# Kernel optimization log

Hardware: AMD Instinct MI355X
Metric: run time of the kernel (lower is better)

The kernel has to match this reference:

```python
import jax, jax.numpy as jnp
import numpy as np

RRELU_SLOPE = (1.0 / 8.0 + 1.0 / 3.0) / 2.0  # F.rrelu deterministic (eval) slope

N_ENTS, H_DIM, R2, T, E = 50000, 200, 500, 4, 400000


def setup_inputs() -> dict:
    key = jax.random.key(0)
    ks = jax.random.split(key, 16)
    s = 0.05
    inp = {
        # learned parameters
        "dynamic_emb": jax.random.normal(ks[0], (N_ENTS, H_DIM), jnp.float32),
        "emb_rel": jax.random.normal(ks[1], (R2, H_DIM), jnp.float32) * s,
        "W_ih": jax.random.normal(ks[2], (3 * H_DIM, 2 * H_DIM), jnp.float32) * s,
        "W_hh": jax.random.normal(ks[3], (3 * H_DIM, H_DIM), jnp.float32) * s,
        "b_ih": jnp.zeros((3 * H_DIM,), jnp.float32),
        "b_hh": jnp.zeros((3 * H_DIM,), jnp.float32),
        "weight_neighbor": jax.random.normal(ks[4], (H_DIM, H_DIM), jnp.float32) * s,
        "time_gate_weight": jax.random.normal(ks[5], (H_DIM, H_DIM), jnp.float32) * s,
        "time_gate_bias": jnp.zeros((H_DIM,), jnp.float32),
        # per-timestep graph structure [T, E]
        "src": jax.random.randint(ks[6], (T, E), 0, N_ENTS, jnp.int32),
        "dst": jax.random.randint(ks[7], (T, E), 0, N_ENTS, jnp.int32),
        "etype": jax.random.randint(ks[8], (T, E), 0, R2, jnp.int32),
        "r_to_e": jax.random.randint(ks[9], (T, E), 0, N_ENTS, jnp.int32),
        "r_seg": jnp.sort(jax.random.randint(ks[10], (T, E), 0, R2, jnp.int32), axis=1),
    }
    return inp


def _l2norm(x):
    # torch F.normalize along dim=1
    return x / jnp.maximum(jnp.linalg.norm(x, axis=1, keepdims=True), 1e-12)


def reference(dynamic_emb, emb_rel, W_ih, W_hh, b_ih, b_hh, weight_neighbor,
              time_gate_weight, time_gate_bias, src, dst, etype, r_to_e, r_seg):
    N, H = dynamic_emb.shape
    R2_ = emb_rel.shape[0]

    def gru(x, hprev):
        gi = x @ W_ih.T + b_ih
        gh = hprev @ W_hh.T + b_hh
        ir, iz, inn = jnp.split(gi, 3, axis=1)
        hr, hz, hn = jnp.split(gh, 3, axis=1)
        r = jax.nn.sigmoid(ir + hr)
        z = jax.nn.sigmoid(iz + hz)
        n = jnp.tanh(inn + r * hn)
        return (1.0 - z) * n + z * hprev

    def rgcn(h, s, d, et):
        # UnionRGCNLayer: msg = (h_src + rel_emb[etype]) @ W_neighbor, sum-agg, 1/deg norm, rrelu
        msg = (h[s] + emb_rel[et]) @ weight_neighbor  # [E, H]
        agg = jax.ops.segment_sum(msg, d, num_segments=N)
        deg = jax.ops.segment_sum(jnp.ones((s.shape[0],), h.dtype), d, num_segments=N)
        norm = jnp.where(deg > 0, 1.0 / jnp.maximum(deg, 1.0), 0.0)
        out = agg * norm[:, None]
        return jnp.where(out >= 0, out, RRELU_SLOPE * out)

    h_init = _l2norm(dynamic_emb)  # layer_norm=True

    def step(carry, g):
        h, h0 = carry
        s, d, et, rte, rseg = g
        # ragged per-relation segment mean of entity embeddings
        temp = h[rte]  # [E, H]
        sums = jax.ops.segment_sum(temp, rseg, num_segments=R2_)
        cnts = jax.ops.segment_sum(jnp.ones((rte.shape[0],), h.dtype), rseg, num_segments=R2_)
        x_input = jnp.where(cnts[:, None] > 0, sums / jnp.maximum(cnts, 1.0)[:, None], 0.0)
        x_cat = jnp.concatenate([emb_rel, x_input], axis=1)  # [R2, 2H]
        h0_new = _l2norm(gru(x_cat, h0))
        cur = _l2norm(rgcn(h, s, d, et))
        tw = jax.nn.sigmoid(h @ time_gate_weight + time_gate_bias)
        h_new = _l2norm(tw * cur + (1.0 - tw) * h)
        return (h_new, h0_new), h_new

    (h_fin, h0_fin), evolve = jax.lax.scan(
        step, (h_init, emb_rel), (src, dst, etype, r_to_e, r_seg))
    return evolve, h0_fin  # evolve: [T, N, H]; h0: [2*num_rels, H]
```

## Files before the change

kernel.cpp:

```cpp
#include <hip/hip_runtime.h>
#include <hip/hip_bf16.h>

using bf16 = __hip_bfloat16;

constexpr int NE  = 50000;
constexpr int H   = 200;
constexpr int R2C = 500;
constexpr int TS  = 4;
constexpr int EC  = 400000;
constexpr float SLOPE = 0.22916666666666666f;
constexpr int NSCAN = (NE + 255) / 256;

constexpr int KP = 224;
constexpr int KS = 7;
constexpr int NT = 13;

constexpr int GNT = 38;
constexpr int GKI = 13;
constexpr int GKH = 7;
constexpr int GR  = 512;
constexpr int GCS = 608;

constexpr int RCH = 64;

#define DEVINL __device__ __forceinline__

typedef __bf16 bf16x8v __attribute__((ext_vector_type(8)));
typedef float  f32x4   __attribute__((ext_vector_type(4)));

DEVINL float b2f(bf16 v) { return __bfloat162float(v); }
DEVINL bf16  f2b(float v) { return __float2bfloat16(v); }
DEVINL unsigned short f2bu(float x) { bf16 b = f2b(x); return *reinterpret_cast<unsigned short*>(&b); }
DEVINL float u2f(unsigned short u) { unsigned int w = (unsigned int)u << 16; float f; __builtin_memcpy(&f, &w, 4); return f; }

DEVINL float wave_sum(float v) {
  #pragma unroll
  for (int o = 32; o > 0; o >>= 1) v += __shfl_xor(v, o, 64);
  return v;
}

DEVINL float sigmoidf(float x) { return 1.0f / (1.0f + expf(-x)); }

__global__ __launch_bounds__(256) void k_init_h(const float* __restrict__ de,
                                                float* __restrict__ h,
                                                unsigned short* __restrict__ hb0) {
  int wid = threadIdx.x >> 6, lane = threadIdx.x & 63;
  int row = blockIdx.x * 4 + wid;
  if (row >= NE) return;
  int d0 = lane * 4;
  bool act = d0 < H;
  float4 v = make_float4(0.f, 0.f, 0.f, 0.f);
  if (act) v = *reinterpret_cast<const float4*>(de + (size_t)row * H + d0);
  float ss = v.x * v.x + v.y * v.y + v.z * v.z + v.w * v.w;
  ss = wave_sum(ss);
  float sc = 1.0f / fmaxf(sqrtf(ss), 1e-12f);
  if (act) {
    float4 o = make_float4(v.x * sc, v.y * sc, v.z * sc, v.w * sc);
    *reinterpret_cast<float4*>(h + (size_t)row * H + d0) = o;
    ushort4 ob; ob.x = f2bu(o.x); ob.y = f2bu(o.y); ob.z = f2bu(o.z); ob.w = f2bu(o.w);
    *reinterpret_cast<ushort4*>(hb0 + (size_t)row * KP + d0) = ob;
  } else if (d0 < KP) {
    ushort4 z; z.x = z.y = z.z = z.w = 0;
    *reinterpret_cast<ushort4*>(hb0 + (size_t)row * KP + d0) = z;
  }
}

__global__ __launch_bounds__(256) void k_init_h0(const float* er, float* h0) {
  int i = blockIdx.x * 256 + threadIdx.x;
  if (i < R2C * H) h0[i] = er[i];
}

__global__ __launch_bounds__(256) void k_relw(const float* er, const float* wn, float* relW) {
  __shared__ float a[H];
  int r = blockIdx.x;
  for (int d = threadIdx.x; d < H; d += 256) a[d] = er[r * H + d];
  __syncthreads();
  for (int c = threadIdx.x; c < H; c += 256) {
    float s = 0.f;
    for (int k = 0; k < H; k++) s += a[k] * wn[k * H + c];
    relW[r * H + c] = s;
  }
}

__global__ __launch_bounds__(256) void k_packb(const float* wn, const float* tg,
                                               unsigned short* bpack) {
  int t = blockIdx.x * 256 + threadIdx.x;
  int total = 2 * NT * KS * 64;
  if (t >= total) return;
  int m    = t / (NT * KS * 64);
  int rem  = t % (NT * KS * 64);
  int nt   = rem / (KS * 64);
  int rem2 = rem % (KS * 64);
  int ks   = rem2 / 64, lane = rem2 % 64;
  const float* W = m ? tg : wn;
  int n = nt * 16 + (lane & 15);
  unsigned short out[8];
  #pragma unroll
  for (int j = 0; j < 8; j++) {
    int k = ks * 32 + (lane >> 4) * 8 + j;
    float v = (k < H && n < H) ? W[k * H + n] : 0.f;
    out[j] = f2bu(v);
  }
  unsigned short* dst = bpack + (size_t)t * 8;
  #pragma unroll
  for (int j = 0; j < 8; j++) dst[j] = out[j];
}

__global__ __launch_bounds__(256) void k_packgru(const float* __restrict__ wih,
                                                 const float* __restrict__ whh,
                                                 unsigned short* __restrict__ bgi,
                                                 unsigned short* __restrict__ bgh) {
  int t = blockIdx.x * 256 + threadIdx.x;
  const int tot_i = GNT * GKI * 64;
  const int tot_h = GNT * GKH * 64;
  if (t < tot_i) {
    int nt = t / (GKI * 64);
    int rem = t % (GKI * 64);
    int ks = rem / 64, lane = rem % 64;
    int n = nt * 16 + (lane & 15);
    unsigned short o[8];
    #pragma unroll
    for (int j = 0; j < 8; j++) {
      int k = ks * 32 + (lane >> 4) * 8 + j;
      o[j] = (n < 3 * H && k < 2 * H) ? f2bu(wih[n * (2 * H) + k]) : (unsigned short)0;
    }
    unsigned short* dstp = bgi + (size_t)t * 8;
    #pragma unroll
    for (int j = 0; j < 8; j++) dstp[j] = o[j];
  } else if (t < tot_i + tot_h) {
    int t2 = t - tot_i;
    int nt = t2 / (GKH * 64);
    int rem = t2 % (GKH * 64);
    int ks = rem / 64, lane = rem % 64;
    int n = nt * 16 + (lane & 15);
    unsigned short o[8];
    #pragma unroll
    for (int j = 0; j < 8; j++) {
      int k = ks * 32 + (lane >> 4) * 8 + j;
      o[j] = (n < 3 * H && k < H) ? f2bu(whh[n * H + k]) : (unsigned short)0;
    }
    unsigned short* dstp = bgh + (size_t)t2 * 8;
    #pragma unroll
    for (int j = 0; j < 8; j++) dstp[j] = o[j];
  }
}

__global__ __launch_bounds__(256) void k_a2b(const float* __restrict__ er,
                                             const float* __restrict__ sums,
                                             const int* __restrict__ segstart,
                                             const float* __restrict__ h0,
                                             unsigned short* __restrict__ xcatb,
                                             unsigned short* __restrict__ h0b) {
  int i = blockIdx.x * 256 + threadIdx.x;
  const int n1 = GR * 416;
  if (i < n1) {
    int r = i / 416, c = i % 416;
    float v = 0.f;
    if (r < R2C) {
      if (c < H) v = er[r * H + c];
      else if (c < 2 * H) {
        int cnt = segstart[r + 1] - segstart[r];
        float inv = cnt > 0 ? 1.0f / (float)cnt : 0.0f;
        v = sums[r * H + (c - H)] * inv;
      }
    }
    xcatb[i] = f2bu(v);
  } else {
    int i2 = i - n1;
    if (i2 < GR * 224) {
      int r = i2 / 224, c = i2 % 224;
      float v = (r < R2C && c < H) ? h0[r * H + c] : 0.f;
      h0b[i2] = f2bu(v);
    }
  }
}

__global__ void k_zero_f(float* p, int n) {
  int i = blockIdx.x * 256 + threadIdx.x;
  if (i < n) p[i] = 0.f;
}
__global__ void k_zero_i(int* p, int n) {
  int i = blockIdx.x * 256 + threadIdx.x;
  if (i < n) p[i] = 0;
}

__global__ __launch_bounds__(512) void k_segbounds4(const int* __restrict__ rseg,
                                                    int* __restrict__ segstart4) {
  const int* rs = rseg + (size_t)blockIdx.x * EC;
  int* out = segstart4 + blockIdx.x * (R2C + 1);
  for (int r = threadIdx.x; r <= R2C; r += 512) {
    int lo = 0, hi = EC;
    while (lo < hi) { int m = (lo + hi) >> 1; if (rs[m] < r) lo = m + 1; else hi = m; }
    out[r] = lo;
  }
}

__global__ void k_hist4(const int* __restrict__ dst, int* __restrict__ deg4) {
  int base = (blockIdx.x * 256 + threadIdx.x) * 4;
  if (base + 3 < TS * EC) {
    int4 d4 = *reinterpret_cast<const int4*>(dst + base);
    int t = base / EC;
    atomicAdd(&deg4[t * NE + d4.x], 1);
    atomicAdd(&deg4[t * NE + d4.y], 1);
    atomicAdd(&deg4[t * NE + d4.z], 1);
    atomicAdd(&deg4[t * NE + d4.w], 1);
  }
}

__global__ __launch_bounds__(256) void k_scan1(const int* __restrict__ deg4,
                                               int* __restrict__ offs4,
                                               int* __restrict__ bsums4) {
  __shared__ int s[256];
  int t = blockIdx.x / NSCAN, blk = blockIdx.x % NSCAN;
  int i = blk * 256 + threadIdx.x;
  int v = (i < NE) ? deg4[t * NE + i] : 0;
  s[threadIdx.x] = v;
  __syncthreads();
  for (int o = 1; o < 256; o <<= 1) {
    int add = (threadIdx.x >= o) ? s[threadIdx.x - o] : 0;
    __syncthreads();
    s[threadIdx.x] += add;
    __syncthreads();
  }
  if (i < NE) offs4[t * (NE + 1) + i] = s[threadIdx.x] - v;
  if (threadIdx.x == 255) bsums4[t * 256 + blk] = s[255];
}

__global__ __launch_bounds__(256) void k_scan2(int* bsums4) {
  __shared__ int s[256];
  int t = blockIdx.x;
  int v = (threadIdx.x < NSCAN) ? bsums4[t * 256 + threadIdx.x] : 0;
  s[threadIdx.x] = v;
  __syncthreads();
  for (int o = 1; o < 256; o <<= 1) {
    int add = (threadIdx.x >= o) ? s[threadIdx.x - o] : 0;
    __syncthreads();
    s[threadIdx.x] += add;
    __syncthreads();
  }
  if (threadIdx.x < NSCAN) bsums4[t * 256 + threadIdx.x] = s[threadIdx.x] - v;
}

__global__ void k_scan3(int* __restrict__ offs4, const int* __restrict__ bsums4,
                        int* __restrict__ cursor4) {
  int t = blockIdx.x / NSCAN, blk = blockIdx.x % NSCAN;
  int i = blk * 256 + threadIdx.x;
  if (i < NE) {
    int o = offs4[t * (NE + 1) + i] + bsums4[t * 256 + blk];
    offs4[t * (NE + 1) + i] = o;
    cursor4[t * NE + i] = o;
  }
  if (blk == 0 && threadIdx.x == 0) offs4[t * (NE + 1) + NE] = EC;
}

__global__ void k_scatter4(const int* __restrict__ dst, const int* __restrict__ src,
                           const int* __restrict__ et, int* __restrict__ cursor4,
                           unsigned int* __restrict__ se4) {
  int base = (blockIdx.x * 256 + threadIdx.x) * 4;
  if (base + 3 < TS * EC) {
    int4 d4 = *reinterpret_cast<const int4*>(dst + base);
    int4 s4 = *reinterpret_cast<const int4*>(src + base);
    int4 e4 = *reinterpret_cast<const int4*>(et + base);
    int t = base / EC;
    int* cur = cursor4 + t * NE;
    unsigned int* se = se4 + (size_t)t * EC;
    int p0 = atomicAdd(&cur[d4.x], 1);
    int p1 = atomicAdd(&cur[d4.y], 1);
    int p2 = atomicAdd(&cur[d4.z], 1);
    int p3 = atomicAdd(&cur[d4.w], 1);
    se[p0] = (unsigned int)s4.x | ((unsigned int)e4.x << 16);
    se[p1] = (unsigned int)s4.y | ((unsigned int)e4.y << 16);
    se[p2] = (unsigned int)s4.z | ((unsigned int)e4.z << 16);
    se[p3] = (unsigned int)s4.w | ((unsigned int)e4.w << 16);
  }
}

__global__ __launch_bounds__(256) void k_relsums(const int* __restrict__ rseg,
                                                 const int* __restrict__ rte,
                                                 const unsigned short* __restrict__ hb,
                                                 float* __restrict__ sums) {
  int base = blockIdx.x * RCH;
  int d = threadIdx.x;
  bool act = d < H;
  float a0 = 0.f, a1 = 0.f, a2 = 0.f, a3 = 0.f;
  int prev = rseg[base];
  for (int g = 0; g < RCH; g += 8) {
    int e = base + g;
    int4 sgA = *reinterpret_cast<const int4*>(rseg + e);
    int4 sgB = *reinterpret_cast<const int4*>(rseg + e + 4);
    int4 rrA = *reinterpret_cast<const int4*>(rte + e);
    int4 rrB = *reinterpret_cast<const int4*>(rte + e + 4);
    if (sgB.w == prev) {
      if (act) {
        float v0 = u2f(hb[(size_t)rrA.x * KP + d]);
        float v1 = u2f(hb[(size_t)rrA.y * KP + d]);
        float v2 = u2f(hb[(size_t)rrA.z * KP + d]);
        float v3 = u2f(hb[(size_t)rrA.w * KP + d]);
        float v4 = u2f(hb[(size_t)rrB.x * KP + d]);
        float v5 = u2f(hb[(size_t)rrB.y * KP + d]);
        float v6 = u2f(hb[(size_t)rrB.z * KP + d]);
        float v7 = u2f(hb[(size_t)rrB.w * KP + d]);
        a0 += v0; a1 += v1; a2 += v2; a3 += v3;
        a0 += v4; a1 += v5; a2 += v6; a3 += v7;
      }
    } else {
      int ss[8] = {sgA.x, sgA.y, sgA.z, sgA.w, sgB.x, sgB.y, sgB.z, sgB.w};
      int rr[8] = {rrA.x, rrA.y, rrA.z, rrA.w, rrB.x, rrB.y, rrB.z, rrB.w};
      #pragma unroll
      for (int j = 0; j < 8; j++) {
        if (ss[j] != prev) {
          if (act) atomicAdd(&sums[prev * H + d], a0 + a1 + a2 + a3);
          a0 = a1 = a2 = a3 = 0.f;
          prev = ss[j];
        }
        if (act) a0 += u2f(hb[(size_t)rr[j] * KP + d]);
      }
    }
  }
  if (act) atomicAdd(&sums[prev * H + d], a0 + a1 + a2 + a3);
}

__global__ __launch_bounds__(256) void k_grumm(const unsigned short* __restrict__ xcatb,
                                               const unsigned short* __restrict__ h0b,
                                               const unsigned short* __restrict__ bgi,
                                               const unsigned short* __restrict__ bgh,
                                               float* __restrict__ gi_ws,
                                               float* __restrict__ gh_ws) {
  int wid = threadIdx.x >> 6, lane = threadIdx.x & 63;
  int nt   = blockIdx.x % GNT;
  int row0 = (blockIdx.x / GNT) * 64 + wid * 16;
  int arow = row0 + (lane & 15);

  const unsigned short* api = xcatb + (size_t)arow * 416 + (lane >> 4) * 8;
  bf16x8v ai[GKI];
  #pragma unroll
  for (int ks = 0; ks < GKI; ks++)
    ai[ks] = *reinterpret_cast<const bf16x8v*>(api + ks * 32);
  const unsigned short* aph = h0b + (size_t)arow * 224 + (lane >> 4) * 8;
  bf16x8v ah[GKH];
  #pragma unroll
  for (int ks = 0; ks < GKH; ks++)
    ah[ks] = *reinterpret_cast<const bf16x8v*>(aph + ks * 32);

  const unsigned short* bip = bgi + ((size_t)(nt * GKI) * 64 + lane) * 8;
  bf16x8v bi[GKI];
  #pragma unroll
  for (int ks = 0; ks < GKI; ks++)
    bi[ks] = *reinterpret_cast<const bf16x8v*>(bip + (size_t)ks * 64 * 8);
  const unsigned short* bhp = bgh + ((size_t)(nt * GKH) * 64 + lane) * 8;
  bf16x8v bh[GKH];
  #pragma unroll
  for (int ks = 0; ks < GKH; ks++)
    bh[ks] = *reinterpret_cast<const bf16x8v*>(bhp + (size_t)ks * 64 * 8);

  f32x4 a1 = {}, a2 = {};
  #pragma unroll
  for (int ks = 0; ks < GKI; ks++)
    a1 = __builtin_amdgcn_mfma_f32_16x16x32_bf16(ai[ks], bi[ks], a1, 0, 0, 0);
  #pragma unroll
  for (int ks = 0; ks < GKH; ks++)
    a2 = __builtin_amdgcn_mfma_f32_16x16x32_bf16(ah[ks], bh[ks], a2, 0, 0, 0);

  int col = nt * 16 + (lane & 15);
  int rb = row0 + (lane >> 4) * 4;
  #pragma unroll
  for (int q = 0; q < 4; q++) {
    gi_ws[(size_t)(rb + q) * GCS + col] = a1[q];
    gh_ws[(size_t)(rb + q) * GCS + col] = a2[q];
  }
}

__global__ __launch_bounds__(256) void k_grutail(const float* __restrict__ gi_ws,
                                                 const float* __restrict__ gh_ws,
                                                 const float* __restrict__ b_ih,
                                                 const float* __restrict__ b_hh,
                                                 float* __restrict__ h0,
                                                 float* __restrict__ h0_out) {
  __shared__ float xc[H];
  __shared__ float red[4];
  int r = blockIdx.x;
  int tid = threadIdx.x, wid = tid >> 6, lane = tid & 63;
  float ssp = 0.f;
  for (int d = tid; d < H; d += 256) {
    float gir = gi_ws[(size_t)r * GCS + d]         + b_ih[d];
    float ghr = gh_ws[(size_t)r * GCS + d]         + b_hh[d];
    float giz = gi_ws[(size_t)r * GCS + H + d]     + b_ih[H + d];
    float ghz = gh_ws[(size_t)r * GCS + H + d]     + b_hh[H + d];
    float gin = gi_ws[(size_t)r * GCS + 2 * H + d] + b_ih[2 * H + d];
    float ghn = gh_ws[(size_t)r * GCS + 2 * H + d] + b_hh[2 * H + d];
    float rg = sigmoidf(gir + ghr);
    float z  = sigmoidf(giz + ghz);
    float n  = tanhf(gin + rg * ghn);
    float hv = h0[r * H + d];
    float o  = (1.0f - z) * n + z * hv;
    xc[d] = o;
    ssp += o * o;
  }
  ssp = wave_sum(ssp);
  if (lane == 0) red[wid] = ssp;
  __syncthreads();
  float ss = red[0] + red[1] + red[2] + red[3];
  float sc = 1.0f / fmaxf(sqrtf(ss), 1e-12f);
  for (int d = tid; d < H; d += 256) {
    float o = xc[d] * sc;
    h0[r * H + d] = o;
    if (h0_out) h0_out[r * H + d] = o;
  }
}

__global__ __launch_bounds__(256) void k_mfma_gemm(const unsigned short* __restrict__ hb,
                                                   const unsigned short* __restrict__ bpack,
                                                   const float* __restrict__ tgb,
                                                   bf16* __restrict__ hWb,
                                                   bf16* __restrict__ twb) {
  int wid = threadIdx.x >> 6, lane = threadIdx.x & 63;
  int row0 = blockIdx.x * 64 + wid * 16;
  if (row0 >= NE) return;
  int arow = min(row0 + (lane & 15), NE - 1);
  const unsigned short* ap = hb + (size_t)arow * KP + (lane >> 4) * 8;
  bf16x8v a[KS];
  #pragma unroll
  for (int ks = 0; ks < KS; ks++)
    a[ks] = *reinterpret_cast<const bf16x8v*>(ap + ks * 32);

  const unsigned short* b1p = bpack + (size_t)lane * 8;
  const unsigned short* b2p = b1p + (size_t)NT * KS * 64 * 8;
  int colb = lane & 15;
  int rbase = row0 + (lane >> 4) * 4;

  for (int nt = 0; nt < NT; nt++) {
    bf16x8v b1[KS], b2[KS];
    #pragma unroll
    for (int ks = 0; ks < KS; ks++) {
      size_t boff = (size_t)(nt * KS + ks) * 64 * 8;
      b1[ks] = *reinterpret_cast<const bf16x8v*>(b1p + boff);
      b2[ks] = *reinterpret_cast<const bf16x8v*>(b2p + boff);
    }
    f32x4 acc1 = {}, acc2 = {};
    #pragma unroll
    for (int ks = 0; ks < KS; ks++) {
      acc1 = __builtin_amdgcn_mfma_f32_16x16x32_bf16(a[ks], b1[ks], acc1, 0, 0, 0);
      acc2 = __builtin_amdgcn_mfma_f32_16x16x32_bf16(a[ks], b2[ks], acc2, 0, 0, 0);
    }
    int col = nt * 16 + colb;
    bool cok = (col < H);
    float bias = cok ? tgb[col] : 0.f;
    #pragma unroll
    for (int q = 0; q < 4; q++) {
      int row = rbase + q;
      if (cok && row < NE) {
        hWb[(size_t)row * H + col] = f2b(acc1[q]);
        twb[(size_t)row * H + col] = f2b(sigmoidf(acc2[q] + bias));
      }
    }
  }
}

__global__ __launch_bounds__(256) void k_aggfin(const int* __restrict__ offs,
                                                const unsigned int* __restrict__ se,
                                                const bf16* __restrict__ hWb,
                                                const float* __restrict__ relW,
                                                const bf16* __restrict__ twb,
                                                float* __restrict__ h,
                                                float* __restrict__ evolve,
                                                unsigned short* __restrict__ hbnext) {
  int wid = threadIdx.x >> 6, lane = threadIdx.x & 63;
  int i = blockIdx.x * 4 + wid;
  if (i >= NE) return;
  int s0 = offs[i], s1 = offs[i + 1];
  int d0 = lane * 4;
  bool act = d0 < H;
  const unsigned short* hw = (const unsigned short*)hWb;
  float a0 = 0.f, a1 = 0.f, a2 = 0.f, a3 = 0.f;

  int p = s0;
  for (; p + 4 <= s1; p += 4) {
    unsigned int e0 = se[p], e1 = se[p + 1], e2 = se[p + 2], e3 = se[p + 3];
    if (act) {
      ushort4 m0 = *reinterpret_cast<const ushort4*>(hw + (size_t)(e0 & 0xFFFFu) * H + d0);
      ushort4 m1 = *reinterpret_cast<const ushort4*>(hw + (size_t)(e1 & 0xFFFFu) * H + d0);
      ushort4 m2 = *reinterpret_cast<const ushort4*>(hw + (size_t)(e2 & 0xFFFFu) * H + d0);
      ushort4 m3 = *reinterpret_cast<const ushort4*>(hw + (size_t)(e3 & 0xFFFFu) * H + d0);
      float4 r0 = *reinterpret_cast<const float4*>(relW + (size_t)(e0 >> 16) * H + d0);
      float4 r1 = *reinterpret_cast<const float4*>(relW + (size_t)(e1 >> 16) * H + d0);
      float4 r2 = *reinterpret_cast<const float4*>(relW + (size_t)(e2 >> 16) * H + d0);
      float4 r3 = *reinterpret_cast<const float4*>(relW + (size_t)(e3 >> 16) * H + d0);
      a0 += u2f(m0.x) + r0.x + u2f(m1.x) + r1.x + u2f(m2.x) + r2.x + u2f(m3.x) + r3.x;
      a1 += u2f(m0.y) + r0.y + u2f(m1.y) + r1.y + u2f(m2.y) + r2.y + u2f(m3.y) + r3.y;
      a2 += u2f(m0.z) + r0.z + u2f(m1.z) + r1.z + u2f(m2.z) + r2.z + u2f(m3.z) + r3.z;
      a3 += u2f(m0.w) + r0.w + u2f(m1.w) + r1.w + u2f(m2.w) + r2.w + u2f(m3.w) + r3.w;
    }
  }
  for (; p < s1; p++) {
    unsigned int e0 = se[p];
    if (act) {
      ushort4 m0 = *reinterpret_cast<const ushort4*>(hw + (size_t)(e0 & 0xFFFFu) * H + d0);
      float4 r0 = *reinterpret_cast<const float4*>(relW + (size_t)(e0 >> 16) * H + d0);
      a0 += u2f(m0.x) + r0.x;
      a1 += u2f(m0.y) + r0.y;
      a2 += u2f(m0.z) + r0.z;
      a3 += u2f(m0.w) + r0.w;
    }
  }

  int deg = s1 - s0;
  float nrm = deg > 0 ? 1.0f / (float)deg : 0.0f;
  float c0 = a0 * nrm; c0 = c0 >= 0.f ? c0 : SLOPE * c0;
  float c1 = a1 * nrm; c1 = c1 >= 0.f ? c1 : SLOPE * c1;
  float c2 = a2 * nrm; c2 = c2 >= 0.f ? c2 : SLOPE * c2;
  float c3 = a3 * nrm; c3 = c3 >= 0.f ? c3 : SLOPE * c3;
  float ss = act ? (c0 * c0 + c1 * c1 + c2 * c2 + c3 * c3) : 0.f;
  ss = wave_sum(ss);
  float sc = 1.0f / fmaxf(sqrtf(ss), 1e-12f);
  c0 *= sc; c1 *= sc; c2 *= sc; c3 *= sc;

  float v0 = 0.f, v1 = 0.f, v2 = 0.f, v3 = 0.f;
  if (act) {
    ushort4 t4 = *reinterpret_cast<const ushort4*>((const unsigned short*)twb + (size_t)i * H + d0);
    float4 hv = *reinterpret_cast<const float4*>(h + (size_t)i * H + d0);
    float t0 = u2f(t4.x), t1 = u2f(t4.y), t2 = u2f(t4.z), t3 = u2f(t4.w);
    v0 = t0 * c0 + (1.0f - t0) * hv.x;
    v1 = t1 * c1 + (1.0f - t1) * hv.y;
    v2 = t2 * c2 + (1.0f - t2) * hv.z;
    v3 = t3 * c3 + (1.0f - t3) * hv.w;
  }
  float ss2 = v0 * v0 + v1 * v1 + v2 * v2 + v3 * v3;
  ss2 = wave_sum(ss2);
  float sc2 = 1.0f / fmaxf(sqrtf(ss2), 1e-12f);
  if (act) {
    float4 o = make_float4(v0 * sc2, v1 * sc2, v2 * sc2, v3 * sc2);
    *reinterpret_cast<float4*>(h + (size_t)i * H + d0) = o;
    *reinterpret_cast<float4*>(evolve + (size_t)i * H + d0) = o;
    if (hbnext) {
      ushort4 ob; ob.x = f2bu(o.x); ob.y = f2bu(o.y); ob.z = f2bu(o.z); ob.w = f2bu(o.w);
      *reinterpret_cast<ushort4*>(hbnext + (size_t)i * KP + d0) = ob;
    }
  } else if (d0 < KP && hbnext) {
    ushort4 z; z.x = z.y = z.z = z.w = 0;
    *reinterpret_cast<ushort4*>(hbnext + (size_t)i * KP + d0) = z;
  }
}

extern "C" void kernel_launch(void* const* d_in, const int* in_sizes, int n_in,
                              void* d_out, int out_size, void* d_ws, size_t ws_size,
                              hipStream_t stream) {
  const float* de  = (const float*)d_in[0];
  const float* er  = (const float*)d_in[1];
  const float* wih = (const float*)d_in[2];
  const float* whh = (const float*)d_in[3];
  const float* bih = (const float*)d_in[4];
  const float* bhh = (const float*)d_in[5];
  const float* wn  = (const float*)d_in[6];
  const float* tg  = (const float*)d_in[7];
  const float* tgb = (const float*)d_in[8];
  const int* src  = (const int*)d_in[9];
  const int* dst  = (const int*)d_in[10];
  const int* et   = (const int*)d_in[11];
  const int* rte  = (const int*)d_in[12];
  const int* rseg = (const int*)d_in[13];

  char* w = (char*)d_ws;
  auto alloc = [&](size_t bytes) -> char* {
    char* p = w;
    w += (bytes + 255) / 256 * 256;
    return p;
  };
  float* h     = (float*)alloc(sizeof(float) * (size_t)NE * H);
  bf16*  hWb   = (bf16*) alloc(sizeof(bf16)  * (size_t)NE * H);
  bf16*  twb   = (bf16*) alloc(sizeof(bf16)  * (size_t)NE * H);
  float* relW  = (float*)alloc(sizeof(float) * R2C * H);
  float* h0    = (float*)alloc(sizeof(float) * R2C * H);
  float* sums  = (float*)alloc(sizeof(float) * R2C * H);
  unsigned short* bpack = (unsigned short*)alloc(sizeof(unsigned short) * 2 * NT * KS * 64 * 8);
  unsigned short* bgi   = (unsigned short*)alloc(sizeof(unsigned short) * GNT * GKI * 64 * 8);
  unsigned short* bgh   = (unsigned short*)alloc(sizeof(unsigned short) * GNT * GKH * 64 * 8);
  unsigned short* xcatb = (unsigned short*)alloc(sizeof(unsigned short) * GR * 416);
  unsigned short* h0b   = (unsigned short*)alloc(sizeof(unsigned short) * GR * 224);
  float* gi_ws = (float*)alloc(sizeof(float) * GR * GCS);
  float* gh_ws = (float*)alloc(sizeof(float) * GR * GCS);
  int* segstart4 = (int*)alloc(sizeof(int) * TS * (R2C + 1));
  int* deg4    = (int*) alloc(sizeof(int) * TS * NE);
  int* offs4   = (int*) alloc(sizeof(int) * TS * (NE + 1));
  int* cursor4 = (int*) alloc(sizeof(int) * TS * NE);
  unsigned int* se4 = (unsigned int*)alloc(sizeof(unsigned int) * (size_t)TS * EC);
  int* bsums4  = (int*) alloc(sizeof(int) * TS * 256);
  (void)ws_size; (void)in_sizes; (void)n_in; (void)out_size;

  float* out    = (float*)d_out;
  float* evolve = out;
  float* h0out  = out + (size_t)TS * NE * H;

  const int gRow4  = (NE + 3) / 4;
  const int gRel   = (R2C * H + 255) / 256;
  const int gPack  = (2 * NT * KS * 64 + 255) / 256;
  const int gPackG = (GNT * (GKI + GKH) * 64 + 255) / 256;
  const int gA2b   = (GR * 416 + GR * 224 + 255) / 256;
  const int gGemm  = (NE + 63) / 64;
  const int gGru   = 8 * GNT;
  const int gRelsum= EC / RCH;
  const int gE4i   = (TS * EC / 4 + 255) / 256;
  const int gZ4    = (TS * NE + 255) / 256;

  k_init_h<<<gRow4, 256, 0, stream>>>(de, h, (unsigned short*)evolve);
  k_init_h0<<<gRel, 256, 0, stream>>>(er, h0);
  k_relw<<<R2C, 256, 0, stream>>>(er, wn, relW);
  k_packb<<<gPack, 256, 0, stream>>>(wn, tg, bpack);
  k_packgru<<<gPackG, 256, 0, stream>>>(wih, whh, bgi, bgh);
  k_segbounds4<<<TS, 512, 0, stream>>>(rseg, segstart4);
  k_zero_i<<<gZ4, 256, 0, stream>>>(deg4, TS * NE);
  k_hist4<<<gE4i, 256, 0, stream>>>(dst, deg4);
  k_scan1<<<TS * NSCAN, 256, 0, stream>>>(deg4, offs4, bsums4);
  k_scan2<<<TS, 256, 0, stream>>>(bsums4);
  k_scan3<<<TS * NSCAN, 256, 0, stream>>>(offs4, bsums4, cursor4);
  k_scatter4<<<gE4i, 256, 0, stream>>>(dst, src, et, cursor4, se4);

  for (int t = 0; t < TS; t++) {
    const int* rseg_t = rseg + (size_t)t * EC;
    const int* rte_t  = rte  + (size_t)t * EC;
    float* evo_t = evolve + (size_t)t * NE * H;
    unsigned short* hb = (unsigned short*)evo_t;
    unsigned short* hbnext = (t < TS - 1) ? (unsigned short*)(evolve + (size_t)(t + 1) * NE * H)
                                          : (unsigned short*)nullptr;

    k_zero_f<<<gRel, 256, 0, stream>>>(sums, R2C * H);
    k_relsums<<<gRelsum, 256, 0, stream>>>(rseg_t, rte_t, hb, sums);
    k_a2b<<<gA2b, 256, 0, stream>>>(er, sums, segstart4 + t * (R2C + 1), h0, xcatb, h0b);
    k_grumm<<<gGru, 256, 0, stream>>>(xcatb, h0b, bgi, bgh, gi_ws, gh_ws);
    k_grutail<<<R2C, 256, 0, stream>>>(gi_ws, gh_ws, bih, bhh,
                                       h0, (t == TS - 1) ? h0out : (float*)nullptr);

    k_mfma_gemm<<<gGemm, 256, 0, stream>>>(hb, bpack, tgb, hWb, twb);

    k_aggfin<<<gRow4, 256, 0, stream>>>(offs4 + t * (NE + 1), se4 + (size_t)t * EC,
                                        hWb, relW, twb, h, evo_t, hbnext);
  }
}
```

Measured before the change: 774.1 us.

## Partition edge scatter by destination range and hoist per-step sums zeroing

The CSR scatter kernel now launches 8 blocks per edge chunk. Each block handles only the edges whose destination falls in its eighth of the node range, so the atomic cursors and output writes of one block stay within a narrower address window and may get better cache locality. In exchange, the edge index arrays are read eight times. Separately, the relation-sum buffer becomes per-timestep and is zeroed once before the loop, which removes four small zeroing launches.

```diff
diff --git a/kernel.cpp b/kernel.cpp
--- a/kernel.cpp
+++ b/kernel.cpp
@@ -22,6 +22,10 @@
 constexpr int GCS = 608;
 
 constexpr int RCH = 64;
+constexpr int NRNG = 8;
+constexpr int DRNG = NE / NRNG;
+constexpr int SCHK = 1024;
+constexpr int NCHK = (EC + SCHK - 1) / SCHK;
 
 #define DEVINL __device__ __forceinline__
 
@@ -253,25 +257,36 @@
   if (blk == 0 && threadIdx.x == 0) offs4[t * (NE + 1) + NE] = EC;
 }
 
-__global__ void k_scatter4(const int* __restrict__ dst, const int* __restrict__ src,
+__global__ void k_scatter8(const int* __restrict__ dst, const int* __restrict__ src,
                            const int* __restrict__ et, int* __restrict__ cursor4,
                            unsigned int* __restrict__ se4) {
-  int base = (blockIdx.x * 256 + threadIdx.x) * 4;
-  if (base + 3 < TS * EC) {
-    int4 d4 = *reinterpret_cast<const int4*>(dst + base);
-    int4 s4 = *reinterpret_cast<const int4*>(src + base);
-    int4 e4 = *reinterpret_cast<const int4*>(et + base);
-    int t = base / EC;
-    int* cur = cursor4 + t * NE;
-    unsigned int* se = se4 + (size_t)t * EC;
-    int p0 = atomicAdd(&cur[d4.x], 1);
-    int p1 = atomicAdd(&cur[d4.y], 1);
-    int p2 = atomicAdd(&cur[d4.z], 1);
-    int p3 = atomicAdd(&cur[d4.w], 1);
-    se[p0] = (unsigned int)s4.x | ((unsigned int)e4.x << 16);
-    se[p1] = (unsigned int)s4.y | ((unsigned int)e4.y << 16);
-    se[p2] = (unsigned int)s4.z | ((unsigned int)e4.z << 16);
-    se[p3] = (unsigned int)s4.w | ((unsigned int)e4.w << 16);
+  int r = blockIdx.x & (NRNG - 1);
+  int rest = blockIdx.x >> 3;
+  int t = rest % TS;
+  int chunk = rest / TS;
+  int li = chunk * SCHK + threadIdx.x * 4;
+  if (li >= EC) return;
+  int base = t * EC + li;
+  int4 d4 = *reinterpret_cast<const int4*>(dst + base);
+  int4 s4 = *reinterpret_cast<const int4*>(src + base);
+  int4 e4 = *reinterpret_cast<const int4*>(et + base);
+  int* cur = cursor4 + t * NE;
+  unsigned int* se = se4 + (size_t)t * EC;
+  if ((unsigned)d4.x / DRNG == (unsigned)r) {
+    int p = atomicAdd(&cur[d4.x], 1);
+    se[p] = (unsigned int)s4.x | ((unsigned int)e4.x << 16);
+  }
+  if ((unsigned)d4.y / DRNG == (unsigned)r) {
+    int p = atomicAdd(&cur[d4.y], 1);
+    se[p] = (unsigned int)s4.y | ((unsigned int)e4.y << 16);
+  }
+  if ((unsigned)d4.z / DRNG == (unsigned)r) {
+    int p = atomicAdd(&cur[d4.z], 1);
+    se[p] = (unsigned int)s4.z | ((unsigned int)e4.z << 16);
+  }
+  if ((unsigned)d4.w / DRNG == (unsigned)r) {
+    int p = atomicAdd(&cur[d4.w], 1);
+    se[p] = (unsigned int)s4.w | ((unsigned int)e4.w << 16);
   }
 }
 
@@ -570,7 +585,7 @@
   bf16*  twb   = (bf16*) alloc(sizeof(bf16)  * (size_t)NE * H);
   float* relW  = (float*)alloc(sizeof(float) * R2C * H);
   float* h0    = (float*)alloc(sizeof(float) * R2C * H);
-  float* sums  = (float*)alloc(sizeof(float) * R2C * H);
+  float* sums4 = (float*)alloc(sizeof(float) * TS * R2C * H);
   unsigned short* bpack = (unsigned short*)alloc(sizeof(unsigned short) * 2 * NT * KS * 64 * 8);
   unsigned short* bgi   = (unsigned short*)alloc(sizeof(unsigned short) * GNT * GKI * 64 * 8);
   unsigned short* bgh   = (unsigned short*)alloc(sizeof(unsigned short) * GNT * GKH * 64 * 8);
@@ -600,6 +615,8 @@
   const int gRelsum= EC / RCH;
   const int gE4i   = (TS * EC / 4 + 255) / 256;
   const int gZ4    = (TS * NE + 255) / 256;
+  const int gZs    = (TS * R2C * H + 255) / 256;
+  const int gScat  = NCHK * TS * NRNG;
 
   k_init_h<<<gRow4, 256, 0, stream>>>(de, h, (unsigned short*)evolve);
   k_init_h0<<<gRel, 256, 0, stream>>>(er, h0);
@@ -607,24 +624,25 @@
   k_packb<<<gPack, 256, 0, stream>>>(wn, tg, bpack);
   k_packgru<<<gPackG, 256, 0, stream>>>(wih, whh, bgi, bgh);
   k_segbounds4<<<TS, 512, 0, stream>>>(rseg, segstart4);
+  k_zero_f<<<gZs, 256, 0, stream>>>(sums4, TS * R2C * H);
   k_zero_i<<<gZ4, 256, 0, stream>>>(deg4, TS * NE);
   k_hist4<<<gE4i, 256, 0, stream>>>(dst, deg4);
   k_scan1<<<TS * NSCAN, 256, 0, stream>>>(deg4, offs4, bsums4);
   k_scan2<<<TS, 256, 0, stream>>>(bsums4);
   k_scan3<<<TS * NSCAN, 256, 0, stream>>>(offs4, bsums4, cursor4);
-  k_scatter4<<<gE4i, 256, 0, stream>>>(dst, src, et, cursor4, se4);
+  k_scatter8<<<gScat, 256, 0, stream>>>(dst, src, et, cursor4, se4);
 
   for (int t = 0; t < TS; t++) {
     const int* rseg_t = rseg + (size_t)t * EC;
     const int* rte_t  = rte  + (size_t)t * EC;
+    float* sums_t = sums4 + (size_t)t * R2C * H;
     float* evo_t = evolve + (size_t)t * NE * H;
     unsigned short* hb = (unsigned short*)evo_t;
     unsigned short* hbnext = (t < TS - 1) ? (unsigned short*)(evolve + (size_t)(t + 1) * NE * H)
                                           : (unsigned short*)nullptr;
 
-    k_zero_f<<<gRel, 256, 0, stream>>>(sums, R2C * H);
-    k_relsums<<<gRelsum, 256, 0, stream>>>(rseg_t, rte_t, hb, sums);
-    k_a2b<<<gA2b, 256, 0, stream>>>(er, sums, segstart4 + t * (R2C + 1), h0, xcatb, h0b);
+    k_relsums<<<gRelsum, 256, 0, stream>>>(rseg_t, rte_t, hb, sums_t);
+    k_a2b<<<gA2b, 256, 0, stream>>>(er, sums_t, segstart4 + t * (R2C + 1), h0, xcatb, h0b);
     k_grumm<<<gGru, 256, 0, stream>>>(xcatb, h0b, bgi, bgh, gi_ws, gh_ws);
     k_grutail<<<R2C, 256, 0, stream>>>(gi_ws, gh_ws, bih, bhh,
                                        h0, (t == TS - 1) ? h0out : (float*)nullptr);
```

Result: faster. 728.8 us (-5.9%).
